# Optimization experiments

Measured on AMD Instinct MI355X. Metric: run time of the kernel, lower is better.

## Reference

```python
import jax, jax.numpy as jnp
import numpy as np

N_NODES = 100000
N_EDGES = 3200000
DIMS = [32, 256, 1024, 1024, 256, 6]


def setup_inputs() -> dict:
    key = jax.random.key(0)
    ks = jax.random.split(key, 2 + 2 * 5)
    inp = {
        "x": jax.random.normal(ks[0], (N_NODES, DIMS[0]), dtype=jnp.float32),
        "edge_index": jax.random.randint(ks[1], (2, N_EDGES), 0, N_NODES, dtype=jnp.int64),
    }
    for i in range(5):
        fan_in, fan_out = DIMS[i], DIMS[i + 1]
        scale = (2.0 / (fan_in + fan_out)) ** 0.5  # glorot-ish
        inp[f"W{i+1}"] = jax.random.normal(ks[2 + 2 * i], (fan_in, fan_out), dtype=jnp.float32) * scale
        inp[f"b{i+1}"] = jnp.zeros((fan_out,), dtype=jnp.float32)
    return inp


def _gcn_forward(x, edge_index, Ws, bs):
    N = x.shape[0]
    # add self loops (PyG GCNConv default)
    loop = jnp.arange(N, dtype=edge_index.dtype)
    src = jnp.concatenate([edge_index[0], loop])
    dst = jnp.concatenate([edge_index[1], loop])
    # symmetric normalization: deg computed on target index (gcn_norm)
    deg = jax.ops.segment_sum(jnp.ones_like(dst, dtype=x.dtype), dst, num_segments=N)
    dinv = jnp.where(deg > 0, jax.lax.rsqrt(deg), 0.0)
    norm = (dinv[src] * dinv[dst])[:, None]  # [E+N, 1]

    def conv(h, W, b):
        h = h @ W                                    # dense linear
        msg = h[src] * norm                          # gather + scale
        agg = jax.ops.segment_sum(msg, dst, num_segments=N)  # scatter-add
        return agg + b

    h = x
    for i in range(4):
        h = jax.nn.relu(conv(h, Ws[i], bs[i]))
    return conv(h, Ws[4], bs[4])


def reference(x, edge_index, W1, b1, W2, b2, W3, b3, W4, b4, W5, b5):
    return _gcn_forward(x, edge_index, (W1, W2, W3, W4, W5), (b1, b2, b3, b4, b5))
```

## Files before the change

### kernel.cpp

```cpp
#include <hip/hip_runtime.h>

typedef unsigned char u8;
typedef unsigned short u16;
typedef unsigned int u32;
typedef __bf16 bf16_t;
typedef bf16_t bf16x8 __attribute__((ext_vector_type(8)));
typedef float f32x4 __attribute__((ext_vector_type(4)));
typedef float f32x2 __attribute__((ext_vector_type(2)));

#define LDS_PTR(p) ((__attribute__((address_space(3))) unsigned int*)(p))
#define GLB_PTR(p) ((const __attribute__((address_space(1))) unsigned int*)(p))

#define BSH 9
#define BCAP 32768

static __device__ __forceinline__ float bf2f(u16 h) {
  u32 u = ((u32)h) << 16;
  return __builtin_bit_cast(float, u);
}
static __device__ __forceinline__ u16 f2bf(float f) {
  u32 u = __builtin_bit_cast(u32, f);
  u += 0x7fffu + ((u >> 16) & 1u);
  return (u16)(u >> 16);
}
static __device__ __forceinline__ void accum_d(float* acc, int j, u32 d, float w) {
  float lo = __builtin_bit_cast(float, d << 16);
  float hi = __builtin_bit_cast(float, d & 0xffff0000u);
  acc[j] += w * lo;
  acc[j + 1] += w * hi;
}

__global__ void detect_kernel(const int* __restrict__ ei, const u16* __restrict__ x,
                              int* __restrict__ flags) {
  __shared__ int cnt;
  if (threadIdx.x == 0) cnt = 0;
  __syncthreads();
  if (blockIdx.x == 0) {
    if (ei[1 + 2 * threadIdx.x] != 0) atomicAdd(&cnt, 1);
    __syncthreads();
    if (threadIdx.x == 0) flags[0] = (cnt == 0) ? 1 : 0;
  } else {
    u32 u = x[threadIdx.x];
    u32 e = (u >> 7) & 0xFF;
    if (e >= 0x60 && e <= 0x83) atomicAdd(&cnt, 1);
    __syncthreads();
    if (threadIdx.x == 0) flags[1] = (cnt >= 240) ? 0 : 1;
  }
}

static __device__ __forceinline__ int eidx(const void* ei, size_t i, int m) {
  return m ? (int)((const long long*)ei)[i] : ((const int*)ei)[i];
}

__global__ void zero_kernel(int* __restrict__ p, int n) {
  int i = blockIdx.x * 256 + threadIdx.x;
  if (i < n) p[i] = 0;
}

__global__ void zero_out_kernel(void* __restrict__ out, int n, const int* __restrict__ flags) {
  int i = blockIdx.x * 256 + threadIdx.x;
  if (i < n) {
    if (flags[1]) ((float*)out)[i] = 0.0f;
    else ((u16*)out)[i] = 0;
  }
}

struct CvtArgs {
  const void* src[10];
  u16* dst[10];
  int K[10];
  int N[10];
  int start[11];
};
__global__ void convert_all_kernel(CvtArgs a, const int* __restrict__ flags) {
  int idx = blockIdx.x * 256 + threadIdx.x;
  int f32 = flags[1];
#pragma unroll
  for (int t = 0; t < 10; ++t) {
    if (idx >= a.start[t] && idx < a.start[t + 1]) {
      int local = idx - a.start[t];
      int K = a.K[t], N = a.N[t];
      int k = local / N, n = local - k * N;
      float v = f32 ? ((const float*)a.src[t])[local] : bf2f(((const u16*)a.src[t])[local]);
      a.dst[t][(size_t)n * K + k] = f2bf(v);
    }
  }
}

__global__ __launch_bounds__(256) void bin_kernel(const void* __restrict__ ei,
                                                  int* __restrict__ gcur,
                                                  int2* __restrict__ pairs, int E, int Nn,
                                                  const int* __restrict__ flags, int nblk) {
  __shared__ int h[256];
  __shared__ int base[256];
  const int m = flags[0];
  const int nb = (Nn + (1 << BSH) - 1) >> BSH;
  const int per = (E + nblk - 1) / nblk;
  const int e0 = blockIdx.x * per;
  const int e1 = (e0 + per < E) ? e0 + per : E;
  for (int i = threadIdx.x; i < nb; i += 256) h[i] = 0;
  __syncthreads();
  for (int e = e0 + threadIdx.x; e < e1; e += 256) {
    int d = eidx(ei, (size_t)E + e, m);
    if ((u32)d < (u32)Nn) atomicAdd(&h[d >> BSH], 1);
  }
  __syncthreads();
  for (int i = threadIdx.x; i < nb; i += 256) {
    base[i] = atomicAdd(&gcur[i], h[i]);
    h[i] = 0;
  }
  __syncthreads();
  for (int e = e0 + threadIdx.x; e < e1; e += 256) {
    int d = eidx(ei, (size_t)E + e, m);
    if ((u32)d >= (u32)Nn) continue;
    int s = eidx(ei, (size_t)e, m);
    if ((u32)s >= (u32)Nn) s = 0;
    int b = d >> BSH;
    int p = base[b] + atomicAdd(&h[b], 1);
    if (p < BCAP) pairs[(size_t)b * BCAP + p] = make_int2(s, d);
  }
}

__global__ __launch_bounds__(256) void bucket_scan_kernel(const int* __restrict__ gcur,
                                                          int* __restrict__ gbase, int NB) {
  __shared__ int sd[256];
  int tid = threadIdx.x;
  int v = (tid < NB) ? gcur[tid] : 0;
  if (v > BCAP) v = BCAP;
  sd[tid] = v;
  __syncthreads();
  for (int s = 1; s < 256; s <<= 1) {
    int t = (tid >= s) ? sd[tid - s] : 0;
    __syncthreads();
    sd[tid] += t;
    __syncthreads();
  }
  if (tid < NB) gbase[tid] = sd[tid] - v;
}

__global__ __launch_bounds__(512) void bucket_finalize_kernel(
    const int2* __restrict__ pairs, const int* __restrict__ gcur,
    const int* __restrict__ gbase, int* __restrict__ rowp, float* __restrict__ dinv,
    int* __restrict__ csr, int Nn) {
  __shared__ int cnt[512];
  __shared__ int scn[512];
  const int b = blockIdx.x;
  const int n0 = b << BSH;
  const int tid = threadIdx.x;
  cnt[tid] = 0;
  __syncthreads();
  int tot = gcur[b];
  if (tot > BCAP) tot = BCAP;
  for (int i = tid; i < tot; i += 512) {
    int2 pr = pairs[(size_t)b * BCAP + i];
    atomicAdd(&cnt[pr.y - n0], 1);
  }
  __syncthreads();
  int myc = cnt[tid];
  scn[tid] = myc;
  __syncthreads();
  for (int s = 1; s < 512; s <<= 1) {
    int t = (tid >= s) ? scn[tid - s] : 0;
    __syncthreads();
    scn[tid] += t;
    __syncthreads();
  }
  const int node = n0 + tid;
  const int start = gbase[b] + scn[tid] - myc;
  if (node < Nn) {
    rowp[node] = start;
    dinv[node] = rsqrtf((float)(myc + 1));
    if (node == Nn - 1) rowp[Nn] = gbase[b] + scn[tid];
  }
  cnt[tid] = start;
  __syncthreads();
  for (int i = tid; i < tot; i += 512) {
    int2 pr = pairs[(size_t)b * BCAP + i];
    int p = atomicAdd(&cnt[pr.y - n0], 1);
    csr[p] = pr.x;
  }
}

template <int W, bool SRCF, bool DSTF>
__global__ __launch_bounds__(256) void spmm_kernel(
    const void* __restrict__ Hb, void* __restrict__ Gb,
    const int* __restrict__ rowp, const int* __restrict__ csr,
    const float* __restrict__ dinv, const u16* __restrict__ bias,
    int relu, int Nn, int src_stride, long long src_coloff,
    int dst_stride, long long dst_coloff, const int* __restrict__ flags) {
  constexpr int B = 16;
  const int lane = threadIdx.x & 63;
  const int node = __builtin_amdgcn_readfirstlane(blockIdx.x * 4 + (threadIdx.x >> 6));
  if (node >= Nn) return;
  const bool act = lane < W;
  const int off = lane;
  int sf32 = 0, of32 = 0;
  if (SRCF) sf32 = flags[1];
  if (DSTF) of32 = flags[1];
  const u16* Hs = (const u16*)Hb;
  float acc = 0.0f;

  auto srcidx = [&](int s) -> size_t {
    return (size_t)src_coloff + (size_t)s * src_stride + off;
  };
  const int e1 = rowp[node + 1];
  int e = rowp[node];
  for (; e + B <= e1; e += B) {
    int s[B];
#pragma unroll
    for (int j = 0; j < B; ++j) s[j] = csr[e + j];
    float wv[B];
#pragma unroll
    for (int j = 0; j < B; ++j) wv[j] = dinv[s[j]];
    float v[B];
#pragma unroll
    for (int j = 0; j < B; ++j) {
      size_t idx = srcidx(s[j]);
      v[j] = act ? ((SRCF && sf32) ? ((const float*)Hb)[idx] : bf2f(Hs[idx])) : 0.0f;
    }
#pragma unroll
    for (int j = 0; j < B; ++j) acc += wv[j] * v[j];
  }
  for (; e < e1; ++e) {
    int s = csr[e];
    if (act) {
      size_t idx = srcidx(s);
      acc += dinv[s] * ((SRCF && sf32) ? ((const float*)Hb)[idx] : bf2f(Hs[idx]));
    }
  }
  const float wi = dinv[node];
  if (act) {
    size_t idx = srcidx(node);
    acc += wi * ((SRCF && sf32) ? ((const float*)Hb)[idx] : bf2f(Hs[idx]));
  }
  if (!act) return;
  float v = acc * wi;
  if (bias) v += bf2f(bias[off]);
  if (relu) v = fmaxf(v, 0.0f);
  size_t didx = (size_t)dst_coloff + (size_t)node * dst_stride + off;
  if (DSTF && of32) ((float*)Gb)[didx] = v;
  else ((u16*)Gb)[didx] = f2bf(v);
}

template <int W>
__global__ __launch_bounds__(256) void spmm_fp8_kernel(
    const u8* __restrict__ Hq, u16* __restrict__ Gout,
    const int* __restrict__ rowp, const int* __restrict__ csr,
    const float* __restrict__ dinv, int n0, int n1, int dst_stride) {
  constexpr int BPL = W / 64;
  constexpr int ND = BPL / 4;
  constexpr int B = (W == 1024) ? 8 : 16;
  const int lane = threadIdx.x & 63;
  const int node = __builtin_amdgcn_readfirstlane(n0 + blockIdx.x * 4 + (threadIdx.x >> 6));
  if (node >= n1) return;
  const int off = lane * BPL;
  f32x2 acc[2 * ND] = {};

  auto dec = [&](const u32* d, float w) {
    f32x2 w2 = {w, w};
#pragma unroll
    for (int q = 0; q < ND; ++q) {
      f32x2 a = __builtin_amdgcn_cvt_pk_f32_fp8((int)d[q], false);
      f32x2 b = __builtin_amdgcn_cvt_pk_f32_fp8((int)d[q], true);
      acc[2 * q] += w2 * a;
      acc[2 * q + 1] += w2 * b;
    }
  };

  const int e1r = rowp[node + 1];
  int e = rowp[node];
  for (; e + B <= e1r; e += B) {
    int s[B];
#pragma unroll
    for (int j = 0; j < B; ++j) s[j] = csr[e + j];
    float wv[B];
#pragma unroll
    for (int j = 0; j < B; ++j) wv[j] = dinv[s[j]];
    u32 v[B][ND];
#pragma unroll
    for (int j = 0; j < B; ++j) {
      const u8* p = Hq + (size_t)s[j] * W + off;
      if constexpr (ND == 4) *(int4*)&v[j][0] = *(const int4*)p;
      else v[j][0] = *(const u32*)p;
    }
#pragma unroll
    for (int j = 0; j < B; ++j) dec(v[j], wv[j]);
  }
  for (; e < e1r; ++e) {
    int s = csr[e];
    u32 v[ND];
    const u8* p = Hq + (size_t)s * W + off;
    if constexpr (ND == 4) *(int4*)&v[0] = *(const int4*)p;
    else v[0] = *(const u32*)p;
    dec(v, dinv[s]);
  }
  const float wi = dinv[node];
  {
    u32 v[ND];
    const u8* p = Hq + (size_t)node * W + off;
    if constexpr (ND == 4) *(int4*)&v[0] = *(const int4*)p;
    else v[0] = *(const u32*)p;
    dec(v, wi);
  }

  u32 d[2 * ND];
#pragma unroll
  for (int k = 0; k < 2 * ND; ++k) {
    float v0 = acc[k].x * wi, v1 = acc[k].y * wi;
    d[k] = (u32)f2bf(v0) | ((u32)f2bf(v1) << 16);
  }
  u16* gp = Gout + (size_t)(node - n0) * dst_stride + off;
  if constexpr (ND == 4) {
    ((int4*)gp)[0] = make_int4((int)d[0], (int)d[1], (int)d[2], (int)d[3]);
    ((int4*)gp)[1] = make_int4((int)d[4], (int)d[5], (int)d[6], (int)d[7]);
  } else {
    *(int2*)gp = make_int2((int)d[0], (int)d[1]);
  }
}

__global__ __launch_bounds__(256) void spmm_i8_kernel(
    const u8* __restrict__ Hq, u16* __restrict__ G,
    const int* __restrict__ rowp, const int* __restrict__ csr,
    const float* __restrict__ dinv, const u32* __restrict__ maxbits,
    const u16* __restrict__ bias, int relu, int Nn, int dst_stride) {
  constexpr int B = 16;
  const int lane = threadIdx.x & 63;
  const int node = __builtin_amdgcn_readfirstlane(blockIdx.x * 4 + (threadIdx.x >> 6));
  if (node >= Nn) return;
  const int off = lane * 4;
  float mx = __builtin_bit_cast(float, *maxbits);
  float sq = mx > 0.0f ? mx * (1.0f / 127.0f) : 0.0f;
  float acc[4] = {};

  auto dec = [&](u32 d, float w) {
    acc[0] += w * (float)(int)(char)(d & 0xff);
    acc[1] += w * (float)(int)(char)((d >> 8) & 0xff);
    acc[2] += w * (float)(int)(char)((d >> 16) & 0xff);
    acc[3] += w * (float)(int)(char)(d >> 24);
  };

  const int e1 = rowp[node + 1];
  int e = rowp[node];
  for (; e + B <= e1; e += B) {
    int s[B];
#pragma unroll
    for (int j = 0; j < B; ++j) s[j] = csr[e + j];
    float wv[B];
#pragma unroll
    for (int j = 0; j < B; ++j) wv[j] = dinv[s[j]];
    u32 v[B];
#pragma unroll
    for (int j = 0; j < B; ++j) v[j] = *(const u32*)(Hq + (size_t)s[j] * 256 + off);
#pragma unroll
    for (int j = 0; j < B; ++j) dec(v[j], wv[j]);
  }
  for (; e < e1; ++e) {
    int s = csr[e];
    dec(*(const u32*)(Hq + (size_t)s * 256 + off), dinv[s]);
  }
  const float wi = dinv[node];
  dec(*(const u32*)(Hq + (size_t)node * 256 + off), wi);

  float vals[4];
#pragma unroll
  for (int k = 0; k < 4; ++k) {
    float v = acc[k] * wi * sq;
    if (bias) v += bf2f(bias[off + k]);
    if (relu) v = fmaxf(v, 0.0f);
    vals[k] = v;
  }
  u32 d0 = (u32)f2bf(vals[0]) | ((u32)f2bf(vals[1]) << 16);
  u32 d1 = (u32)f2bf(vals[2]) | ((u32)f2bf(vals[3]) << 16);
  *(int2*)(G + (size_t)node * dst_stride + off) = make_int2((int)d0, (int)d1);
}

__global__ void quant_kernel(const u16* __restrict__ t4, u8* __restrict__ t4q,
                             const u32* __restrict__ maxbits, int n4) {
  int i = blockIdx.x * 256 + threadIdx.x;
  if (i >= n4) return;
  float mx = __builtin_bit_cast(float, *maxbits);
  float inv = mx > 0.0f ? 127.0f / mx : 0.0f;
  int2 v = ((const int2*)t4)[i];
  float f0 = bf2f((u16)(v.x & 0xffff)), f1 = bf2f((u16)((u32)v.x >> 16));
  float f2 = bf2f((u16)(v.y & 0xffff)), f3 = bf2f((u16)((u32)v.y >> 16));
  int q0 = (int)rintf(f0 * inv), q1 = (int)rintf(f1 * inv);
  int q2 = (int)rintf(f2 * inv), q3 = (int)rintf(f3 * inv);
  q0 = min(127, max(-127, q0)); q1 = min(127, max(-127, q1));
  q2 = min(127, max(-127, q2)); q3 = min(127, max(-127, q3));
  ((u32*)t4q)[i] = (u32)(q0 & 0xff) | ((u32)(q1 & 0xff) << 8) |
                   ((u32)(q2 & 0xff) << 16) | ((u32)(q3 & 0xff) << 24);
}

__global__ __launch_bounds__(256) void gemm_fast_kernel(
    const u16* __restrict__ A, int lda, const u16* __restrict__ Bt,
    u16* __restrict__ C, int ldc, const u16* __restrict__ bias,
    int M, int N, int K, int relu, int fp8out, u32* __restrict__ maxout) {
  __shared__ __align__(16) u16 sA[128 * 64];
  __shared__ __align__(16) u16 sB[128 * 64];
  const int tid = threadIdx.x;
  const int lane = tid & 63;
  const int wave = __builtin_amdgcn_readfirstlane(tid >> 6);
  const int m0 = blockIdx.y * 128, n0 = blockIdx.x * 128;
  const int wm = (wave & 1) * 64, wn = (wave >> 1) * 64;
  const int lr = lane & 15, lq = lane >> 4;
  const int lrow = lane >> 3;
  const int lcol = (lane & 7) * 8;
  f32x4 acc[4][4] = {};

  for (int kb = 0; kb < K; kb += 64) {
#pragma unroll
    for (int it = 0; it < 4; ++it) {
      const int rbase = (it * 4 + wave) * 8;
      int gm = m0 + rbase + lrow;
      if (gm >= M) gm = M - 1;
      __builtin_amdgcn_global_load_lds(GLB_PTR(A + (size_t)gm * lda + kb + lcol),
                                       LDS_PTR(sA + rbase * 64), 16, 0, 0);
      const int gn = n0 + rbase + lrow;
      __builtin_amdgcn_global_load_lds(GLB_PTR(Bt + (size_t)gn * K + kb + lcol),
                                       LDS_PTR(sB + rbase * 64), 16, 0, 0);
    }
    __syncthreads();
#pragma unroll
    for (int ks = 0; ks < 2; ++ks) {
      bf16x8 af[4], bfr[4];
#pragma unroll
      for (int i = 0; i < 4; ++i)
        af[i] = *(const bf16x8*)(sA + (wm + i * 16 + lr) * 64 + ks * 32 + lq * 8);
#pragma unroll
      for (int i = 0; i < 4; ++i)
        bfr[i] = *(const bf16x8*)(sB + (wn + i * 16 + lr) * 64 + ks * 32 + lq * 8);
#pragma unroll
      for (int im = 0; im < 4; ++im)
#pragma unroll
        for (int in = 0; in < 4; ++in)
          acc[im][in] = __builtin_amdgcn_mfma_f32_16x16x32_bf16(af[im], bfr[in], acc[im][in], 0, 0, 0);
    }
    __syncthreads();
  }
  u32 mymax = 0;
#pragma unroll
  for (int im = 0; im < 4; ++im) {
#pragma unroll
    for (int in = 0; in < 4; ++in) {
      int col = n0 + wn + in * 16 + lr;
      float bv = bias ? bf2f(bias[col]) : 0.0f;
#pragma unroll
      for (int r = 0; r < 4; ++r) {
        int row = m0 + wm + im * 16 + lq * 4 + r;
        if (row < M) {
          float v = acc[im][in][r] + bv;
          if (relu) v = fmaxf(v, 0.0f);
          if (maxout) {
            u32 ab = __builtin_bit_cast(u32, v) & 0x7fffffffu;
            mymax = mymax > ab ? mymax : ab;
          }
          if (fp8out) {
            int pk = __builtin_amdgcn_cvt_pk_fp8_f32(v, v, 0, false);
            ((u8*)C)[(size_t)row * ldc + col] = (u8)(pk & 0xff);
          } else {
            C[(size_t)row * ldc + col] = f2bf(v);
          }
        }
      }
    }
  }
  if (maxout) {
    u32* red = (u32*)sA;
    red[tid] = mymax;
    __syncthreads();
    for (int s = 128; s > 0; s >>= 1) {
      if (tid < s) red[tid] = red[tid] > red[tid + s] ? red[tid] : red[tid + s];
      __syncthreads();
    }
    if (tid == 0) atomicMax(maxout, red[0]);
  }
}

#define LP 72
__global__ __launch_bounds__(256) void gemm_small_kernel(
    const u16* __restrict__ A, int lda, const u16* __restrict__ Bt,
    u16* __restrict__ C, int ldc, const u16* __restrict__ bias,
    int M, int N, int K, int relu, int fp8out) {
  __shared__ __align__(16) u16 sA[128 * LP];
  __shared__ __align__(16) u16 sB[128 * LP];
  const int tid = threadIdx.x;
  const int lane = tid & 63, wave = tid >> 6;
  const int m0 = blockIdx.y * 128, n0 = blockIdx.x * 128;
  const int wm = (wave & 1) * 64, wn = (wave >> 1) * 64;
  const int lr = lane & 15;
  const int lq = lane >> 4;
  f32x4 acc[4][4] = {};

  for (int kb = 0; kb < K; kb += 64) {
#pragma unroll
    for (int it = 0; it < 4; ++it) {
      int linear = it * 2048 + tid * 8;
      int row = linear >> 6, kc = linear & 63;
      int gm = m0 + row, gk = kb + kc;
      int4 v = make_int4(0, 0, 0, 0);
      if (gm < M && gk < K) v = *(const int4*)(A + (size_t)gm * lda + gk);
      *(int4*)(sA + row * LP + kc) = v;
    }
#pragma unroll
    for (int it = 0; it < 4; ++it) {
      int linear = it * 2048 + tid * 8;
      int row = linear >> 6, kc = linear & 63;
      int gn = n0 + row, gk = kb + kc;
      int4 v = make_int4(0, 0, 0, 0);
      if (gn < N && gk < K) v = *(const int4*)(Bt + (size_t)gn * K + gk);
      *(int4*)(sB + row * LP + kc) = v;
    }
    __syncthreads();
#pragma unroll
    for (int ks = 0; ks < 2; ++ks) {
      bf16x8 af[4], bfr[4];
#pragma unroll
      for (int i = 0; i < 4; ++i)
        af[i] = *(const bf16x8*)(sA + (wm + i * 16 + lr) * LP + ks * 32 + lq * 8);
#pragma unroll
      for (int i = 0; i < 4; ++i)
        bfr[i] = *(const bf16x8*)(sB + (wn + i * 16 + lr) * LP + ks * 32 + lq * 8);
#pragma unroll
      for (int im = 0; im < 4; ++im)
#pragma unroll
        for (int in = 0; in < 4; ++in)
          acc[im][in] = __builtin_amdgcn_mfma_f32_16x16x32_bf16(af[im], bfr[in], acc[im][in], 0, 0, 0);
    }
    __syncthreads();
  }
#pragma unroll
  for (int im = 0; im < 4; ++im) {
#pragma unroll
    for (int in = 0; in < 4; ++in) {
      int col = n0 + wn + in * 16 + lr;
      if (col >= N) continue;
      float bv = bias ? bf2f(bias[col]) : 0.0f;
#pragma unroll
      for (int r = 0; r < 4; ++r) {
        int row = m0 + wm + im * 16 + lq * 4 + r;
        if (row < M) {
          float v = acc[im][in][r] + bv;
          if (relu) v = fmaxf(v, 0.0f);
          if (fp8out) {
            int pk = __builtin_amdgcn_cvt_pk_fp8_f32(v, v, 0, false);
            ((u8*)C)[(size_t)row * ldc + col] = (u8)(pk & 0xff);
          } else {
            C[(size_t)row * ldc + col] = f2bf(v);
          }
        }
      }
    }
  }
}

extern "C" void kernel_launch(void* const* d_in, const int* in_sizes, int n_in,
                              void* d_out, int out_size, void* d_ws, size_t ws_size,
                              hipStream_t stream) {
  const u16* x  = (const u16*)d_in[0];
  const int* ei = (const int*)d_in[1];

  const int Nn = in_sizes[0] / 32;
  const int E  = in_sizes[1] / 2;
  const int CH = (Nn + 7) / 8;
  const int NR = (Nn + CH - 1) / CH;
  const int NB = (Nn + (1 << BSH) - 1) >> BSH;

  char* w = (char*)d_ws;
  size_t off = 0;
  auto alloc = [&](size_t bytes) -> void* {
    void* p = w + off;
    off = (off + bytes + 255) & ~(size_t)255;
    return p;
  };
  int*   flags  = (int*)alloc(256);
  int*   gcur   = (int*)alloc(1024);
  int*   gbase  = (int*)alloc(1024);
  u32*   tmax   = (u32*)alloc(256);
  int*   rowp   = (int*)alloc((size_t)(Nn + 1) * 4);
  float* dinv   = (float*)alloc((size_t)Nn * 4);
  int*   csr    = (int*)alloc((size_t)E * 4);
  u16*   Wt1    = (u16*)alloc((size_t)32 * 256 * 2);
  u16*   Wt2    = (u16*)alloc((size_t)256 * 1024 * 2);
  u16*   Wt3    = (u16*)alloc((size_t)1024 * 1024 * 2);
  u16*   Wt4    = (u16*)alloc((size_t)1024 * 256 * 2);
  u16*   Wt5    = (u16*)alloc((size_t)256 * 6 * 2);
  u16*   bc1    = (u16*)alloc(256 * 2);
  u16*   bc2    = (u16*)alloc(1024 * 2);
  u16*   bc3    = (u16*)alloc(1024 * 2);
  u16*   bc4    = (u16*)alloc(256 * 2);
  u16*   bc5    = (u16*)alloc(6 * 2);
  size_t selems = (size_t)CH * 1024;
  u16*   S      = (u16*)alloc(selems * 2);
  u16*   H      = (u16*)alloc((size_t)Nn * 1024 * 2);
  const size_t required = off;
  (void)n_in;

  if (ws_size < required) {
    if (ws_size >= 4096) {
      detect_kernel<<<2, 256, 0, stream>>>(ei, x, flags);
      zero_out_kernel<<<(out_size + 255) / 256, 256, 0, stream>>>(d_out, out_size, flags);
    }
    return;
  }

  u8*  h2q = (u8*)H;
  u8*  t4q = (u8*)H;
  u16* g2  = H + (size_t)Nn * 512;
  u16* t4  = H + (size_t)Nn * 512;
  u8*  h1q = (u8*)(H + (size_t)Nn * 768);
  u16* h3R = H + (size_t)Nn * 768;
  u16* h4  = H + (size_t)Nn * 768;

  int2* pairs = (int2*)H;

  detect_kernel<<<2, 256, 0, stream>>>(ei, x, flags);
  zero_kernel<<<3, 256, 0, stream>>>(gcur, 576);
  bin_kernel<<<1024, 256, 0, stream>>>(ei, gcur, pairs, E, Nn, flags, 1024);
  bucket_scan_kernel<<<1, 256, 0, stream>>>(gcur, gbase, NB);
  bucket_finalize_kernel<<<NB, 512, 0, stream>>>(pairs, gcur, gbase, rowp, dinv, csr, Nn);

  {
    CvtArgs a;
    const int Ks[10] = {32, 1, 256, 1, 1024, 1, 1024, 1, 256, 1};
    const int Ns[10] = {256, 256, 1024, 1024, 1024, 1024, 256, 256, 6, 6};
    u16* ds[10] = {Wt1, bc1, Wt2, bc2, Wt3, bc3, Wt4, bc4, Wt5, bc5};
    int cum = 0;
    for (int t = 0; t < 10; ++t) {
      a.src[t] = d_in[2 + t];
      a.dst[t] = ds[t];
      a.K[t] = Ks[t];
      a.N[t] = Ns[t];
      a.start[t] = cum;
      cum += Ks[t] * Ns[t];
    }
    a.start[10] = cum;
    convert_all_kernel<<<(cum + 255) / 256, 256, 0, stream>>>(a, flags);
  }

  const int sg = (Nn + 3) / 4;
  const int mb = (Nn + 127) / 128;

  spmm_kernel<32, true, false><<<sg, 256, 0, stream>>>(x, S, rowp, csr, dinv, nullptr, 0, Nn,
                                                       32, 0, 32, 0, flags);
  gemm_small_kernel<<<dim3(2, mb), 256, 0, stream>>>(S, 32, Wt1, (u16*)h1q, 256, bc1,
                                                     Nn, 256, 32, 1, 1);

  spmm_fp8_kernel<256><<<sg, 256, 0, stream>>>(h1q, g2, rowp, csr, dinv, 0, Nn, 256);
  gemm_fast_kernel<<<dim3(8, mb), 256, 0, stream>>>(g2, 256, Wt2, (u16*)h2q, 1024, bc2,
                                                    Nn, 1024, 256, 1, 1, nullptr);

  for (int R = 0; R < NR; ++R) {
    int n0 = R * CH;
    int n1 = n0 + CH < Nn ? n0 + CH : Nn;
    int MR = n1 - n0;
    int mbr = (MR + 127) / 128;
    spmm_fp8_kernel<1024><<<(MR + 3) / 4, 256, 0, stream>>>(h2q, S, rowp, csr, dinv, n0, n1, 1024);
    gemm_fast_kernel<<<dim3(8, mbr), 256, 0, stream>>>(S, 1024, Wt3, h3R, 1024, bc3,
                                                       MR, 1024, 1024, 1, 0, nullptr);
    gemm_fast_kernel<<<dim3(2, mbr), 256, 0, stream>>>(h3R, 1024, Wt4, t4 + (size_t)n0 * 256, 256,
                                                       nullptr, MR, 256, 1024, 0, 0, tmax);
  }

  quant_kernel<<<(Nn * 64 + 255) / 256, 256, 0, stream>>>(t4, t4q, tmax, Nn * 64);

  spmm_i8_kernel<<<sg, 256, 0, stream>>>(t4q, h4, rowp, csr, dinv, tmax, bc4, 1, Nn, 256);

  gemm_small_kernel<<<dim3(1, mb), 256, 0, stream>>>(h4, 256, Wt5, S, 6, nullptr,
                                                     Nn, 6, 256, 0, 0);
  spmm_kernel<6, false, true><<<sg, 256, 0, stream>>>(S, d_out, rowp, csr, dinv, bc5, 0, Nn,
                                                      6, 0, 6, 0, flags);
}
```

Measured before the change: 2.186 ms.

## Pack multiple nodes per wavefront in narrow SpMMs and use offset-u8 quantization

The narrow-width SpMM kernels (32 and 6 columns) now pack 2 or 8 destination nodes into each 64-lane wavefront instead of one node per wave, so far fewer lanes sit idle. Neighbour loops become predicated batches with a per-lane edge count. The int8 layer-4 aggregation switches to unsigned offset-128 encoding, using an unsigned byte-to-float convert plus a weight-sum correction instead of sign extension. The zero kernel is folded into the detect kernel as a third block. Packing nodes adds lane divergence when neighbouring nodes have different degrees.

Measured after the change: 2.104 ms. -3.7%, faster.

```diff
diff --git a/kernel.cpp b/kernel.cpp
--- a/kernel.cpp
+++ b/kernel.cpp
@@ -23,15 +23,9 @@
   u += 0x7fffu + ((u >> 16) & 1u);
   return (u16)(u >> 16);
 }
-static __device__ __forceinline__ void accum_d(float* acc, int j, u32 d, float w) {
-  float lo = __builtin_bit_cast(float, d << 16);
-  float hi = __builtin_bit_cast(float, d & 0xffff0000u);
-  acc[j] += w * lo;
-  acc[j + 1] += w * hi;
-}
 
 __global__ void detect_kernel(const int* __restrict__ ei, const u16* __restrict__ x,
-                              int* __restrict__ flags) {
+                              int* __restrict__ flags, int* __restrict__ zp, int zn) {
   __shared__ int cnt;
   if (threadIdx.x == 0) cnt = 0;
   __syncthreads();
@@ -39,22 +33,19 @@
     if (ei[1 + 2 * threadIdx.x] != 0) atomicAdd(&cnt, 1);
     __syncthreads();
     if (threadIdx.x == 0) flags[0] = (cnt == 0) ? 1 : 0;
-  } else {
+  } else if (blockIdx.x == 1) {
     u32 u = x[threadIdx.x];
     u32 e = (u >> 7) & 0xFF;
     if (e >= 0x60 && e <= 0x83) atomicAdd(&cnt, 1);
     __syncthreads();
     if (threadIdx.x == 0) flags[1] = (cnt >= 240) ? 0 : 1;
+  } else {
+    for (int i = threadIdx.x; i < zn; i += 256) zp[i] = 0;
   }
 }
 
 static __device__ __forceinline__ int eidx(const void* ei, size_t i, int m) {
   return m ? (int)((const long long*)ei)[i] : ((const int*)ei)[i];
-}
-
-__global__ void zero_kernel(int* __restrict__ p, int n) {
-  int i = blockIdx.x * 256 + threadIdx.x;
-  if (i < n) p[i] = 0;
 }
 
 __global__ void zero_out_kernel(void* __restrict__ out, int n, const int* __restrict__ flags) {
@@ -181,63 +172,59 @@
   }
 }
 
-template <int W, bool SRCF, bool DSTF>
-__global__ __launch_bounds__(256) void spmm_kernel(
+template <int NPW, int ACT, bool SRCF, bool DSTF>
+__global__ __launch_bounds__(256) void spmm_narrow_kernel(
     const void* __restrict__ Hb, void* __restrict__ Gb,
     const int* __restrict__ rowp, const int* __restrict__ csr,
     const float* __restrict__ dinv, const u16* __restrict__ bias,
-    int relu, int Nn, int src_stride, long long src_coloff,
-    int dst_stride, long long dst_coloff, const int* __restrict__ flags) {
+    int relu, int Nn, int src_stride, int dst_stride, const int* __restrict__ flags) {
+  constexpr int G = 64 / NPW;
   constexpr int B = 16;
   const int lane = threadIdx.x & 63;
-  const int node = __builtin_amdgcn_readfirstlane(blockIdx.x * 4 + (threadIdx.x >> 6));
-  if (node >= Nn) return;
-  const bool act = lane < W;
-  const int off = lane;
+  const int col = lane & (G - 1);
+  const int node = blockIdx.x * 4 * NPW + (threadIdx.x >> 6) * NPW + (lane / G);
+  const bool anode = node < Nn;
+  const bool act = anode && (col < ACT);
   int sf32 = 0, of32 = 0;
   if (SRCF) sf32 = flags[1];
   if (DSTF) of32 = flags[1];
   const u16* Hs = (const u16*)Hb;
+  const float* Hf = (const float*)Hb;
+
+  int e0 = 0, cnt = 0;
+  if (anode) {
+    e0 = rowp[node];
+    cnt = rowp[node + 1] - e0;
+  }
   float acc = 0.0f;
-
-  auto srcidx = [&](int s) -> size_t {
-    return (size_t)src_coloff + (size_t)s * src_stride + off;
-  };
-  const int e1 = rowp[node + 1];
-  int e = rowp[node];
-  for (; e + B <= e1; e += B) {
+  for (int jb = 0; jb < cnt; jb += B) {
     int s[B];
-#pragma unroll
-    for (int j = 0; j < B; ++j) s[j] = csr[e + j];
     float wv[B];
 #pragma unroll
-    for (int j = 0; j < B; ++j) wv[j] = dinv[s[j]];
+    for (int j = 0; j < B; ++j) {
+      bool val = (jb + j) < cnt;
+      s[j] = val ? csr[e0 + jb + j] : node;
+      wv[j] = val ? dinv[s[j]] : 0.0f;
+    }
     float v[B];
 #pragma unroll
     for (int j = 0; j < B; ++j) {
-      size_t idx = srcidx(s[j]);
-      v[j] = act ? ((SRCF && sf32) ? ((const float*)Hb)[idx] : bf2f(Hs[idx])) : 0.0f;
+      size_t idx = (size_t)s[j] * src_stride + col;
+      v[j] = act ? ((SRCF && sf32) ? Hf[idx] : bf2f(Hs[idx])) : 0.0f;
     }
 #pragma unroll
     for (int j = 0; j < B; ++j) acc += wv[j] * v[j];
   }
-  for (; e < e1; ++e) {
-    int s = csr[e];
-    if (act) {
-      size_t idx = srcidx(s);
-      acc += dinv[s] * ((SRCF && sf32) ? ((const float*)Hb)[idx] : bf2f(Hs[idx]));
-    }
-  }
+  if (!act) return;
   const float wi = dinv[node];
-  if (act) {
-    size_t idx = srcidx(node);
-    acc += wi * ((SRCF && sf32) ? ((const float*)Hb)[idx] : bf2f(Hs[idx]));
-  }
-  if (!act) return;
+  {
+    size_t idx = (size_t)node * src_stride + col;
+    acc += wi * ((SRCF && sf32) ? Hf[idx] : bf2f(Hs[idx]));
+  }
   float v = acc * wi;
-  if (bias) v += bf2f(bias[off]);
+  if (bias) v += bf2f(bias[col]);
   if (relu) v = fmaxf(v, 0.0f);
-  size_t didx = (size_t)dst_coloff + (size_t)node * dst_stride + off;
+  size_t didx = (size_t)node * dst_stride + col;
   if (DSTF && of32) ((float*)Gb)[didx] = v;
   else ((u16*)Gb)[didx] = f2bf(v);
 }
@@ -318,7 +305,7 @@
   }
 }
 
-__global__ __launch_bounds__(256) void spmm_i8_kernel(
+__global__ __launch_bounds__(256) void spmm_u8_kernel(
     const u8* __restrict__ Hq, u16* __restrict__ G,
     const int* __restrict__ rowp, const int* __restrict__ csr,
     const float* __restrict__ dinv, const u32* __restrict__ maxbits,
@@ -331,12 +318,14 @@
   float mx = __builtin_bit_cast(float, *maxbits);
   float sq = mx > 0.0f ? mx * (1.0f / 127.0f) : 0.0f;
   float acc[4] = {};
+  float wsum = 0.0f;
 
   auto dec = [&](u32 d, float w) {
-    acc[0] += w * (float)(int)(char)(d & 0xff);
-    acc[1] += w * (float)(int)(char)((d >> 8) & 0xff);
-    acc[2] += w * (float)(int)(char)((d >> 16) & 0xff);
-    acc[3] += w * (float)(int)(char)(d >> 24);
+    acc[0] += w * (float)(d & 0xffu);
+    acc[1] += w * (float)((d >> 8) & 0xffu);
+    acc[2] += w * (float)((d >> 16) & 0xffu);
+    acc[3] += w * (float)(d >> 24);
+    wsum += w;
   };
 
   const int e1 = rowp[node + 1];
@@ -364,7 +353,7 @@
   float vals[4];
 #pragma unroll
   for (int k = 0; k < 4; ++k) {
-    float v = acc[k] * wi * sq;
+    float v = (acc[k] - 128.0f * wsum) * wi * sq;
     if (bias) v += bf2f(bias[off + k]);
     if (relu) v = fmaxf(v, 0.0f);
     vals[k] = v;
@@ -385,10 +374,9 @@
   float f2 = bf2f((u16)(v.y & 0xffff)), f3 = bf2f((u16)((u32)v.y >> 16));
   int q0 = (int)rintf(f0 * inv), q1 = (int)rintf(f1 * inv);
   int q2 = (int)rintf(f2 * inv), q3 = (int)rintf(f3 * inv);
-  q0 = min(127, max(-127, q0)); q1 = min(127, max(-127, q1));
-  q2 = min(127, max(-127, q2)); q3 = min(127, max(-127, q3));
-  ((u32*)t4q)[i] = (u32)(q0 & 0xff) | ((u32)(q1 & 0xff) << 8) |
-                   ((u32)(q2 & 0xff) << 16) | ((u32)(q3 & 0xff) << 24);
+  q0 = min(127, max(-127, q0)) + 128; q1 = min(127, max(-127, q1)) + 128;
+  q2 = min(127, max(-127, q2)) + 128; q3 = min(127, max(-127, q3)) + 128;
+  ((u32*)t4q)[i] = (u32)q0 | ((u32)q1 << 8) | ((u32)q2 << 16) | ((u32)q3 << 24);
 }
 
 __global__ __launch_bounds__(256) void gemm_fast_kernel(
@@ -597,7 +585,7 @@
 
   if (ws_size < required) {
     if (ws_size >= 4096) {
-      detect_kernel<<<2, 256, 0, stream>>>(ei, x, flags);
+      detect_kernel<<<3, 256, 0, stream>>>(ei, x, flags, gcur, 576);
       zero_out_kernel<<<(out_size + 255) / 256, 256, 0, stream>>>(d_out, out_size, flags);
     }
     return;
@@ -613,8 +601,7 @@
 
   int2* pairs = (int2*)H;
 
-  detect_kernel<<<2, 256, 0, stream>>>(ei, x, flags);
-  zero_kernel<<<3, 256, 0, stream>>>(gcur, 576);
+  detect_kernel<<<3, 256, 0, stream>>>(ei, x, flags, gcur, 576);
   bin_kernel<<<1024, 256, 0, stream>>>(ei, gcur, pairs, E, Nn, flags, 1024);
   bucket_scan_kernel<<<1, 256, 0, stream>>>(gcur, gbase, NB);
   bucket_finalize_kernel<<<NB, 512, 0, stream>>>(pairs, gcur, gbase, rowp, dinv, csr, Nn);
@@ -640,8 +627,8 @@
   const int sg = (Nn + 3) / 4;
   const int mb = (Nn + 127) / 128;
 
-  spmm_kernel<32, true, false><<<sg, 256, 0, stream>>>(x, S, rowp, csr, dinv, nullptr, 0, Nn,
-                                                       32, 0, 32, 0, flags);
+  spmm_narrow_kernel<2, 32, true, false><<<(Nn + 7) / 8, 256, 0, stream>>>(
+      x, S, rowp, csr, dinv, nullptr, 0, Nn, 32, 32, flags);
   gemm_small_kernel<<<dim3(2, mb), 256, 0, stream>>>(S, 32, Wt1, (u16*)h1q, 256, bc1,
                                                      Nn, 256, 32, 1, 1);
 
@@ -663,10 +650,10 @@
 
   quant_kernel<<<(Nn * 64 + 255) / 256, 256, 0, stream>>>(t4, t4q, tmax, Nn * 64);
 
-  spmm_i8_kernel<<<sg, 256, 0, stream>>>(t4q, h4, rowp, csr, dinv, tmax, bc4, 1, Nn, 256);
+  spmm_u8_kernel<<<sg, 256, 0, stream>>>(t4q, h4, rowp, csr, dinv, tmax, bc4, 1, Nn, 256);
 
   gemm_small_kernel<<<dim3(1, mb), 256, 0, stream>>>(h4, 256, Wt5, S, 6, nullptr,
                                                      Nn, 6, 256, 0, 0);
-  spmm_kernel<6, false, true><<<sg, 256, 0, stream>>>(S, d_out, rowp, csr, dinv, bc5, 0, Nn,
-                                                      6, 0, 6, 0, flags);
-}
+  spmm_narrow_kernel<8, 6, false, true><<<(Nn + 31) / 32, 256, 0, stream>>>(
+      S, d_out, rowp, csr, dinv, bc5, 0, Nn, 6, 6, flags);
+}
```
